# Optimization experiments

Hardware: AMD Instinct MI355X
Metric: run time of the kernel (lower is better)

## Reference

```python
import jax, jax.numpy as jnp
import numpy as np

B, Q, G = 32, 16384, 128   # batch, num queries, (padded) num GT per image
K = 32                      # first top-k (nearest candidates per GT)
N = 9                       # second top-k (highest-IoU matches per GT)


def box_cxcywh_to_xyxy(b):
    cx, cy, w, h = jnp.split(b, 4, axis=-1)
    return jnp.concatenate([cx - 0.5 * w, cy - 0.5 * h,
                            cx + 0.5 * w, cy + 0.5 * h], axis=-1)


def box_iou(a, b):
    # a, b: broadcastable [..., 4] in xyxy
    lt = jnp.maximum(a[..., :2], b[..., :2])
    rb = jnp.minimum(a[..., 2:], b[..., 2:])
    wh = jnp.clip(rb - lt, 0.0)
    inter = wh[..., 0] * wh[..., 1]
    area_a = (a[..., 2] - a[..., 0]) * (a[..., 3] - a[..., 1])
    area_b = (b[..., 2] - b[..., 0]) * (b[..., 3] - b[..., 1])
    return inter / (area_a + area_b - inter)


def _assign(gt, pred):
    # gt: [G,4] cxcywh, pred: [Q,4] cxcywh
    # euclidean cdist in cxcywh space: [G, Q]
    d = jnp.sqrt(jnp.sum((gt[:, None, :] - pred[None, :, :]) ** 2, axis=-1))
    # k nearest predictions per GT (smallest distance)
    _, kidx = jax.lax.top_k(-d, K)            # [G, K]
    k_boxes = pred[kidx]                       # [G, K, 4]
    iou = box_iou(box_cxcywh_to_xyxy(gt)[:, None, :],
                  box_cxcywh_to_xyxy(k_boxes))           # [G, K]
    vals, ns = jax.lax.top_k(iou, N)           # [G, N] highest IoU among the K
    pred_idx = jnp.take_along_axis(kidx, ns, axis=1)      # [G, N] global pred ids
    gt_idx = jnp.broadcast_to(jnp.arange(gt.shape[0])[:, None], ns.shape)
    return pred_idx.reshape(-1), gt_idx.reshape(-1)


def setup_inputs() -> dict:
    key = jax.random.key(0)
    k1, k2 = jax.random.split(key)
    pred_boxes = jax.random.uniform(k1, (B, Q, 4), dtype=jnp.float32)
    gt_boxes = jax.random.uniform(k2, (B, G, 4), dtype=jnp.float32)
    return {"pred_boxes": pred_boxes, "gt_boxes": gt_boxes}


def reference(pred_boxes, gt_boxes):
    # per-image assignment, vectorized over the batch
    pred_idx, gt_idx = jax.vmap(_assign)(gt_boxes, pred_boxes)
    # pred_idx, gt_idx: [B, G*N] int32 (analog of the list of (i, j) index tensors)
    return pred_idx, gt_idx
```

## Files before the change

### kernel.cpp

```cpp
#include <hip/hip_runtime.h>

#define BB 32
#define QQ 16384
#define GG 128
#define KK 32
#define NN 9
#define TT 16
#define TH 1024
#define RR (QQ / TH)
#define NW (TH / 64)
#define CAP 192
#define ACAP 96
#define UF 4

typedef unsigned long long u64;
typedef unsigned int u32;

#define INFF __uint_as_float(0x7F800000u)

__device__ __forceinline__ u64 pack_asc(float key, u32 idx) {
  return (((u64)__float_as_uint(key)) << 32) | (u64)idx;
}

__device__ __forceinline__ float dist2_ref(const float4 g, const float4 p) {
#pragma clang fp contract(off)
  float dx = g.x - p.x;
  float dy = g.y - p.y;
  float dz = g.z - p.z;
  float dw = g.w - p.w;
  float s = dx * dx + dy * dy;
  s = s + dz * dz;
  s = s + dw * dw;
  return s;
}

__device__ __forceinline__ float iou_ref(const float4 g, const float4 p) {
#pragma clang fp contract(off)
  float gx1 = g.x - 0.5f * g.z, gy1 = g.y - 0.5f * g.w;
  float gx2 = g.x + 0.5f * g.z, gy2 = g.y + 0.5f * g.w;
  float px1 = p.x - 0.5f * p.z, py1 = p.y - 0.5f * p.w;
  float px2 = p.x + 0.5f * p.z, py2 = p.y + 0.5f * p.w;
  float ltx = fmaxf(gx1, px1), lty = fmaxf(gy1, py1);
  float rbx = fminf(gx2, px2), rby = fminf(gy2, py2);
  float wx = fmaxf(rbx - ltx, 0.0f), wy = fmaxf(rby - lty, 0.0f);
  float inter = wx * wy;
  float aa = (gx2 - gx1) * (gy2 - gy1);
  float ab = (px2 - px1) * (py2 - py1);
  return inter / ((aa + ab) - inter);
}

__device__ __forceinline__ u32 f2ord(float f) {
  u32 b = __float_as_uint(f);
  return (b & 0x80000000u) ? ~b : (b | 0x80000000u);
}
__device__ __forceinline__ float ord2f(u32 k) {
  return __uint_as_float((k & 0x80000000u) ? (k & 0x7FFFFFFFu) : ~k);
}

__global__ __launch_bounds__(TH, 4) void atss_kernel(
    const float4* __restrict__ pred, const float4* __restrict__ gtb,
    int* __restrict__ out) {
  __shared__ float smin[TT][TH];
  __shared__ float ckey[TT][CAP];
  __shared__ unsigned short cidx[TT][CAP];
  __shared__ unsigned short sact[TT][ACAP];
  __shared__ int kidx[TT][KK];

  const int t = threadIdx.x;
  const int f = blockIdx.x;
  const int b = (f & 7) * 4 + (f >> 6);
  const int g0 = ((f >> 3) & 7) * TT;

  float4 G[TT];
#pragma unroll
  for (int gg = 0; gg < TT; ++gg) G[gg] = gtb[b * GG + g0 + gg];

  const float4* pb = pred + (size_t)b * QQ;

  float mn[TT];
#pragma unroll
  for (int gg = 0; gg < TT; ++gg) mn[gg] = INFF;

  float4 P[UF];
#pragma unroll
  for (int u = 0; u < UF; ++u) P[u] = pb[t + u * TH];
#pragma unroll
  for (int j = 0; j < RR; j += UF) {
    float4 C[UF];
#pragma unroll
    for (int u = 0; u < UF; ++u) C[u] = P[u];
    if (j + UF < RR) {
#pragma unroll
      for (int u = 0; u < UF; ++u) P[u] = pb[t + (j + UF + u) * TH];
    }
#pragma unroll
    for (int u = 0; u < UF; ++u) {
      float4 p = C[u];
      float pp = fmaf(p.x, p.x, fmaf(p.y, p.y, fmaf(p.z, p.z, p.w * p.w)));
      float qx = p.x + p.x, qy = p.y + p.y, qz = p.z + p.z, qw = p.w + p.w;
#pragma unroll
      for (int gg = 0; gg < TT; ++gg) {
        float acc = fmaf(-G[gg].x, qx, pp);
        acc = fmaf(-G[gg].y, qy, acc);
        acc = fmaf(-G[gg].z, qz, acc);
        acc = fmaf(-G[gg].w, qw, acc);
        mn[gg] = fminf(mn[gg], acc);
      }
    }
  }
#pragma unroll
  for (int gg = 0; gg < TT; ++gg) smin[gg][t] = mn[gg];

  __syncthreads();

  const int w = t >> 6;
  const int lane = t & 63;
  const u64 below = (lane == 0) ? 0ull : ((1ull << lane) - 1ull);

  const float4 gt = gtb[b * GG + g0 + w];

  float V[NW];
#pragma unroll
  for (int k = 0; k < NW; ++k) V[k] = smin[w][lane + 64 * k];

  float m1 = INFF, m2 = INFF;
#pragma unroll
  for (int k = 0; k < NW; ++k) {
    float v = V[k];
    float nm1 = fminf(m1, v);
    m2 = fminf(m2, fmaxf(m1, v));
    m1 = nm1;
  }

  u32 k1 = f2ord(m1), k2 = f2ord(m2);
  u32 pref = 0;
#pragma unroll
  for (int bit = 31; bit >= 0; --bit) {
    u32 tr = pref | (1u << bit);
    int c = __popcll(__ballot(k1 < tr)) + __popcll(__ballot(k2 < tr));
    if (c < 32) pref = tr;
  }
  float Us = ord2f(pref);

  float gg2 = fmaf(gt.x, gt.x,
              fmaf(gt.y, gt.y, fmaf(gt.z, gt.z, gt.w * gt.w)));
  const float sUs = Us + fabsf(Us) * 2e-5f + 4e-6f;
  const float T = fmaxf(Us + gg2, 0.0f) * 1.00002f + 4e-6f;

  int na = 0;
#pragma unroll
  for (int k = 0; k < NW; ++k) {
    bool c = V[k] <= sUs;
    u64 mask = __ballot(c);
    if (c) {
      int pos = na + __popcll(mask & below);
      if (pos < ACAP) sact[w][pos] = (unsigned short)(lane + 64 * k);
    }
    na += __popcll(mask);
  }

  int nCand = 0;
  if (na <= ACAP) {
    const int eo = (lane & 15) * TH;
    const int e0 = lane >> 4;
    const int trips = (na + 15) >> 4;

#define ISSUE(ENT, VV, II, PP)                        \
  {                                                   \
    int ent_ = (ENT);                                 \
    VV = ent_ < na;                                   \
    int ecl_ = VV ? ent_ : 0;                         \
    II = (int)sact[w][ecl_] + eo;                     \
    PP = pb[II];                                      \
  }
#define PROCESS(VV, II, PP)                           \
  {                                                   \
    float d2_ = dist2_ref(gt, PP);                    \
    bool acc_ = VV && (d2_ <= T);                     \
    u64 mask_ = __ballot(acc_);                       \
    if (acc_) {                                       \
      int pos_ = nCand + __popcll(mask_ & below);     \
      if (pos_ < CAP) {                               \
        ckey[w][pos_] = d2_;                          \
        cidx[w][pos_] = (unsigned short)II;           \
      }                                               \
    }                                                 \
    nCand += __popcll(mask_);                         \
  }

    bool va, vb, vc, vd;
    int ia, ib, ic, id;
    float4 pa, pbx, pc, pd;
    ISSUE(e0, va, ia, pa);
    ISSUE(e0 + 4, vb, ib, pbx);
    ISSUE(e0 + 8, vc, ic, pc);
    ISSUE(e0 + 12, vd, id, pd);
    for (int tr = 0; tr < trips; ++tr) {
      int en = e0 + 16 * (tr + 1);
      bool nva, nvb, nvc, nvd;
      int nia, nib, nic, nid;
      float4 npa, npb, npc, npd;
      ISSUE(en, nva, nia, npa);
      ISSUE(en + 4, nvb, nib, npb);
      ISSUE(en + 8, nvc, nic, npc);
      ISSUE(en + 12, nvd, nid, npd);
      PROCESS(va, ia, pa);
      PROCESS(vb, ib, pbx);
      PROCESS(vc, ic, pc);
      PROCESS(vd, id, pd);
      va = nva; ia = nia; pa = npa;
      vb = nvb; ib = nib; pbx = npb;
      vc = nvc; ic = nic; pc = npc;
      vd = nvd; id = nid; pd = npd;
    }
#undef ISSUE
#undef PROCESS
  } else {
    for (int rr = 0; rr < NW; ++rr) {
      int r = lane + 64 * rr;
      for (int j = 0; j < RR; ++j) {
        int i = r + j * TH;
        float d2 = dist2_ref(gt, pb[i]);
        bool acc = d2 <= T;
        u64 mask = __ballot(acc);
        if (acc) {
          int pos = nCand + __popcll(mask & below);
          if (pos < CAP) {
            ckey[w][pos] = d2;
            cidx[w][pos] = (unsigned short)i;
          }
        }
        nCand += __popcll(mask);
      }
    }
  }
  const int n = nCand;

  int selIdx = 0;
  if (n <= 64) {
    bool valid = lane < n;
    float myd = valid ? sqrtf(ckey[w][lane]) : 0.0f;
    u32 myi = valid ? (u32)cidx[w][lane] : 0u;
    u64 mk = valid ? pack_asc(myd, myi) : ~0ull;
    int rank = 0;
    for (int i = 0; i < n; ++i) {
      u64 ki = __shfl(mk, i, 64);
      rank += (ki < mk) ? 1 : 0;
    }
    selIdx = __builtin_amdgcn_ds_permute(rank << 2, (int)myi);
  } else if (n <= CAP) {
    volatile float* vk = ckey[w];
    for (int sel = 0; sel < KK; ++sel) {
      u64 lm = ~0ull;
      int ls = -1;
      for (int s = lane; s < n; s += 64) {
        float d = sqrtf(vk[s]);
        u64 pk = pack_asc(d, (u32)cidx[w][s]);
        if (pk < lm) {
          lm = pk;
          ls = s;
        }
      }
      u64 ww = lm;
#pragma unroll
      for (int j = 32; j > 0; j >>= 1) {
        u64 o = __shfl_xor(ww, j, 64);
        ww = o < ww ? o : ww;
      }
      if (lm == ww && ls >= 0) {
        vk[ls] = INFF;
        kidx[w][sel] = (int)(ww & 0xFFFFFFFFull);
      }
    }
    selIdx = kidx[w][lane & 31];
  } else {
    if (lane == 0) {
      u64 best[KK];
      for (int l = 0; l < KK; ++l) best[l] = ~0ull;
      for (int i = 0; i < QQ; ++i) {
        float d = sqrtf(dist2_ref(gt, pb[i]));
        u64 pk = pack_asc(d, (u32)i);
        if (pk < best[KK - 1]) {
          int pos = KK - 1;
          while (pos > 0 && best[pos - 1] > pk) {
            best[pos] = best[pos - 1];
            --pos;
          }
          best[pos] = pk;
        }
      }
      for (int l = 0; l < KK; ++l) kidx[w][l] = (int)(best[l] & 0xFFFFFFFFull);
    }
    selIdx = kidx[w][lane & 31];
  }

  {
    float iou = 0.0f;
    u32 pi = 0;
    if (lane < KK) {
      pi = (u32)selIdx;
      iou = iou_ref(gt, pb[pi]);
    }
    u32 ik = (lane < KK) ? ~__float_as_uint(iou) : 0xFFFFFFFFu;
    int r9 = 0;
    for (int i = 0; i < KK; ++i) {
      u32 ki = __shfl(ik, i, 64);
      r9 += ((ki < ik) || (ki == ik && i < lane)) ? 1 : 0;
    }
    if (lane < KK && r9 < NN) {
      int base = (b * GG + g0 + w) * NN + r9;
      out[base] = (int)pi;
      out[BB * GG * NN + base] = g0 + w;
    }
  }
}

extern "C" void kernel_launch(void* const* d_in, const int* in_sizes, int n_in,
                              void* d_out, int out_size, void* d_ws, size_t ws_size,
                              hipStream_t stream) {
  (void)in_sizes;
  (void)n_in;
  (void)out_size;
  (void)d_ws;
  (void)ws_size;
  const float4* pred = (const float4*)d_in[0];
  const float4* gt = (const float4*)d_in[1];
  int* out = (int*)d_out;
  atss_kernel<<<(GG / TT) * BB, TH, 0, stream>>>(pred, gt, out);
}
```

Before: 81.40 us.

## Split fused kernel into range-min pass and per-GT selection pass via workspace

Splits the single fused kernel into two launches. Phase 1 uses twice as many blocks, each covering half of the query ranges, and writes per-range minimum distances to a global workspace. Phase 2 runs one 64-thread block per GT and does the threshold search, candidate gathering and top-k selection. The aim is better occupancy and more parallel work during the selection stage, in exchange for a workspace round trip through global memory and a second kernel launch.

```diff
diff --git a/kernel.cpp b/kernel.cpp
--- a/kernel.cpp
+++ b/kernel.cpp
@@ -7,8 +7,9 @@
 #define NN 9
 #define TT 16
 #define TH 1024
-#define RR (QQ / TH)
-#define NW (TH / 64)
+#define HR 8
+#define NRANGE 2048
+#define RPL 32
 #define CAP 192
 #define ACAP 96
 #define UF 4
@@ -57,25 +58,22 @@
   return __uint_as_float((k & 0x80000000u) ? (k & 0x7FFFFFFFu) : ~k);
 }
 
-__global__ __launch_bounds__(TH, 4) void atss_kernel(
+__global__ __launch_bounds__(TH, 8) void atss_phase1(
     const float4* __restrict__ pred, const float4* __restrict__ gtb,
-    int* __restrict__ out) {
-  __shared__ float smin[TT][TH];
-  __shared__ float ckey[TT][CAP];
-  __shared__ unsigned short cidx[TT][CAP];
-  __shared__ unsigned short sact[TT][ACAP];
-  __shared__ int kidx[TT][KK];
-
+    float* __restrict__ ws) {
   const int t = threadIdx.x;
   const int f = blockIdx.x;
-  const int b = (f & 7) * 4 + (f >> 6);
-  const int g0 = ((f >> 3) & 7) * TT;
+  const int b = (f & 7) * 4 + (f >> 7);
+  const int m = (f >> 3) & 7;
+  const int h = (f >> 6) & 1;
+  const int g0 = m * TT;
 
   float4 G[TT];
 #pragma unroll
   for (int gg = 0; gg < TT; ++gg) G[gg] = gtb[b * GG + g0 + gg];
 
   const float4* pb = pred + (size_t)b * QQ;
+  const int r = h * 1024 + t;
 
   float mn[TT];
 #pragma unroll
@@ -83,15 +81,15 @@
 
   float4 P[UF];
 #pragma unroll
-  for (int u = 0; u < UF; ++u) P[u] = pb[t + u * TH];
-#pragma unroll
-  for (int j = 0; j < RR; j += UF) {
+  for (int u = 0; u < UF; ++u) P[u] = pb[r + u * NRANGE];
+#pragma unroll
+  for (int j = 0; j < HR; j += UF) {
     float4 C[UF];
 #pragma unroll
     for (int u = 0; u < UF; ++u) C[u] = P[u];
-    if (j + UF < RR) {
-#pragma unroll
-      for (int u = 0; u < UF; ++u) P[u] = pb[t + (j + UF + u) * TH];
+    if (j + UF < HR) {
+#pragma unroll
+      for (int u = 0; u < UF; ++u) P[u] = pb[r + (j + UF + u) * NRANGE];
     }
 #pragma unroll
     for (int u = 0; u < UF; ++u) {
@@ -108,24 +106,46 @@
       }
     }
   }
-#pragma unroll
-  for (int gg = 0; gg < TT; ++gg) smin[gg][t] = mn[gg];
-
-  __syncthreads();
-
-  const int w = t >> 6;
-  const int lane = t & 63;
+  float* seg = ws + (size_t)((b * 8 + m) * TT) * NRANGE;
+#pragma unroll
+  for (int gg = 0; gg < TT; ++gg) seg[gg * NRANGE + r] = mn[gg];
+}
+
+__global__ __launch_bounds__(64, 4) void atss_phase2(
+    const float4* __restrict__ pred, const float4* __restrict__ gtb,
+    const float* __restrict__ ws, int* __restrict__ out) {
+  __shared__ float ckey[CAP];
+  __shared__ unsigned short cidx[CAP];
+  __shared__ unsigned short sact[ACAP];
+  __shared__ int kidx[KK];
+
+  const int lane = threadIdx.x;
+  const int f = blockIdx.x;
+  const int x = f & 7;
+  const int j = f >> 3;
+  const int b = x * 4 + (j & 3);
+  const int g = j >> 2;
   const u64 below = (lane == 0) ? 0ull : ((1ull << lane) - 1ull);
 
-  const float4 gt = gtb[b * GG + g0 + w];
-
-  float V[NW];
-#pragma unroll
-  for (int k = 0; k < NW; ++k) V[k] = smin[w][lane + 64 * k];
+  const float4 gt = gtb[b * GG + g];
+  const float4* pb = pred + (size_t)b * QQ;
+  const float* vsrc =
+      ws + (size_t)((b * 8 + (g >> 4)) * TT + (g & 15)) * NRANGE;
+
+  float V[RPL];
+  const float4* v4 = (const float4*)(vsrc + lane * RPL);
+#pragma unroll
+  for (int u = 0; u < RPL / 4; ++u) {
+    float4 q = v4[u];
+    V[4 * u + 0] = q.x;
+    V[4 * u + 1] = q.y;
+    V[4 * u + 2] = q.z;
+    V[4 * u + 3] = q.w;
+  }
 
   float m1 = INFF, m2 = INFF;
 #pragma unroll
-  for (int k = 0; k < NW; ++k) {
+  for (int k = 0; k < RPL; ++k) {
     float v = V[k];
     float nm1 = fminf(m1, v);
     m2 = fminf(m2, fmaxf(m1, v));
@@ -149,28 +169,28 @@
 
   int na = 0;
 #pragma unroll
-  for (int k = 0; k < NW; ++k) {
+  for (int k = 0; k < RPL; ++k) {
     bool c = V[k] <= sUs;
     u64 mask = __ballot(c);
     if (c) {
       int pos = na + __popcll(mask & below);
-      if (pos < ACAP) sact[w][pos] = (unsigned short)(lane + 64 * k);
+      if (pos < ACAP) sact[pos] = (unsigned short)(lane * RPL + k);
     }
     na += __popcll(mask);
   }
 
   int nCand = 0;
   if (na <= ACAP) {
-    const int eo = (lane & 15) * TH;
-    const int e0 = lane >> 4;
-    const int trips = (na + 15) >> 4;
+    const int eo = (lane & 7) * NRANGE;
+    const int e0 = lane >> 3;
+    const int trips = (na + 31) >> 5;
 
 #define ISSUE(ENT, VV, II, PP)                        \
   {                                                   \
     int ent_ = (ENT);                                 \
     VV = ent_ < na;                                   \
     int ecl_ = VV ? ent_ : 0;                         \
-    II = (int)sact[w][ecl_] + eo;                     \
+    II = (int)sact[ecl_] + eo;                        \
     PP = pb[II];                                      \
   }
 #define PROCESS(VV, II, PP)                           \
@@ -181,8 +201,8 @@
     if (acc_) {                                       \
       int pos_ = nCand + __popcll(mask_ & below);     \
       if (pos_ < CAP) {                               \
-        ckey[w][pos_] = d2_;                          \
-        cidx[w][pos_] = (unsigned short)II;           \
+        ckey[pos_] = d2_;                             \
+        cidx[pos_] = (unsigned short)II;              \
       }                                               \
     }                                                 \
     nCand += __popcll(mask_);                         \
@@ -192,18 +212,18 @@
     int ia, ib, ic, id;
     float4 pa, pbx, pc, pd;
     ISSUE(e0, va, ia, pa);
-    ISSUE(e0 + 4, vb, ib, pbx);
-    ISSUE(e0 + 8, vc, ic, pc);
-    ISSUE(e0 + 12, vd, id, pd);
+    ISSUE(e0 + 8, vb, ib, pbx);
+    ISSUE(e0 + 16, vc, ic, pc);
+    ISSUE(e0 + 24, vd, id, pd);
     for (int tr = 0; tr < trips; ++tr) {
-      int en = e0 + 16 * (tr + 1);
+      int en = e0 + 32 * (tr + 1);
       bool nva, nvb, nvc, nvd;
       int nia, nib, nic, nid;
       float4 npa, npb, npc, npd;
       ISSUE(en, nva, nia, npa);
-      ISSUE(en + 4, nvb, nib, npb);
-      ISSUE(en + 8, nvc, nic, npc);
-      ISSUE(en + 12, nvd, nid, npd);
+      ISSUE(en + 8, nvb, nib, npb);
+      ISSUE(en + 16, nvc, nic, npc);
+      ISSUE(en + 24, nvd, nid, npd);
       PROCESS(va, ia, pa);
       PROCESS(vb, ib, pbx);
       PROCESS(vc, ic, pc);
@@ -216,18 +236,18 @@
 #undef ISSUE
 #undef PROCESS
   } else {
-    for (int rr = 0; rr < NW; ++rr) {
-      int r = lane + 64 * rr;
-      for (int j = 0; j < RR; ++j) {
-        int i = r + j * TH;
+    for (int rr = 0; rr < RPL; ++rr) {
+      int r = lane * RPL + rr;
+      for (int jj = 0; jj < HR; ++jj) {
+        int i = r + jj * NRANGE;
         float d2 = dist2_ref(gt, pb[i]);
         bool acc = d2 <= T;
         u64 mask = __ballot(acc);
         if (acc) {
           int pos = nCand + __popcll(mask & below);
           if (pos < CAP) {
-            ckey[w][pos] = d2;
-            cidx[w][pos] = (unsigned short)i;
+            ckey[pos] = d2;
+            cidx[pos] = (unsigned short)i;
           }
         }
         nCand += __popcll(mask);
@@ -239,8 +259,8 @@
   int selIdx = 0;
   if (n <= 64) {
     bool valid = lane < n;
-    float myd = valid ? sqrtf(ckey[w][lane]) : 0.0f;
-    u32 myi = valid ? (u32)cidx[w][lane] : 0u;
+    float myd = valid ? sqrtf(ckey[lane]) : 0.0f;
+    u32 myi = valid ? (u32)cidx[lane] : 0u;
     u64 mk = valid ? pack_asc(myd, myi) : ~0ull;
     int rank = 0;
     for (int i = 0; i < n; ++i) {
@@ -249,13 +269,13 @@
     }
     selIdx = __builtin_amdgcn_ds_permute(rank << 2, (int)myi);
   } else if (n <= CAP) {
-    volatile float* vk = ckey[w];
+    volatile float* vk = ckey;
     for (int sel = 0; sel < KK; ++sel) {
       u64 lm = ~0ull;
       int ls = -1;
       for (int s = lane; s < n; s += 64) {
         float d = sqrtf(vk[s]);
-        u64 pk = pack_asc(d, (u32)cidx[w][s]);
+        u64 pk = pack_asc(d, (u32)cidx[s]);
         if (pk < lm) {
           lm = pk;
           ls = s;
@@ -263,16 +283,16 @@
       }
       u64 ww = lm;
 #pragma unroll
-      for (int j = 32; j > 0; j >>= 1) {
-        u64 o = __shfl_xor(ww, j, 64);
+      for (int jx = 32; jx > 0; jx >>= 1) {
+        u64 o = __shfl_xor(ww, jx, 64);
         ww = o < ww ? o : ww;
       }
       if (lm == ww && ls >= 0) {
         vk[ls] = INFF;
-        kidx[w][sel] = (int)(ww & 0xFFFFFFFFull);
-      }
-    }
-    selIdx = kidx[w][lane & 31];
+        kidx[sel] = (int)(ww & 0xFFFFFFFFull);
+      }
+    }
+    selIdx = kidx[lane & 31];
   } else {
     if (lane == 0) {
       u64 best[KK];
@@ -289,9 +309,9 @@
           best[pos] = pk;
         }
       }
-      for (int l = 0; l < KK; ++l) kidx[w][l] = (int)(best[l] & 0xFFFFFFFFull);
-    }
-    selIdx = kidx[w][lane & 31];
+      for (int l = 0; l < KK; ++l) kidx[l] = (int)(best[l] & 0xFFFFFFFFull);
+    }
+    selIdx = kidx[lane & 31];
   }
 
   {
@@ -308,9 +328,9 @@
       r9 += ((ki < ik) || (ki == ik && i < lane)) ? 1 : 0;
     }
     if (lane < KK && r9 < NN) {
-      int base = (b * GG + g0 + w) * NN + r9;
+      int base = (b * GG + g) * NN + r9;
       out[base] = (int)pi;
-      out[BB * GG * NN + base] = g0 + w;
+      out[BB * GG * NN + base] = g;
     }
   }
 }
@@ -321,10 +341,11 @@
   (void)in_sizes;
   (void)n_in;
   (void)out_size;
-  (void)d_ws;
   (void)ws_size;
   const float4* pred = (const float4*)d_in[0];
   const float4* gt = (const float4*)d_in[1];
   int* out = (int*)d_out;
-  atss_kernel<<<(GG / TT) * BB, TH, 0, stream>>>(pred, gt, out);
-}
+  float* ws = (float*)d_ws;
+  atss_phase1<<<512, TH, 0, stream>>>(pred, gt, ws);
+  atss_phase2<<<4096, 64, 0, stream>>>(pred, gt, ws, out);
+}
```

Result: slower. 94.54 us (+16.1%).
